# Optimization experiments

Hardware: AMD Instinct MI355X
Metric: run time of the kernel (lower is better)

The kernel has to match this reference:

```python
import jax, jax.numpy as jnp
import numpy as np

M, K, N = 4096, 7168, 18432  # tokens, in_features, out_features


def setup_inputs() -> dict:
    key = jax.random.key(0)
    kx, kw, ks = jax.random.split(key, 3)
    x = jax.random.normal(kx, (M, K), dtype=jnp.float32)
    # int8 quantized weight, layout [in_features, out_features] as in the torch module
    weight = jax.random.randint(kw, (K, N), -128, 128, dtype=jnp.int8)
    # per-output-channel dequant scale (bf16 in the original; fp32 here for a stable baseline)
    scale = jax.random.uniform(ks, (N,), dtype=jnp.float32) * 0.02 + 1e-3
    return {"x": x, "weight": weight, "scale": scale}


def reference(x, weight, scale):
    # Fused dequant + GEMM: y = x @ (int8_weight * scale_per_out_channel)
    w = weight.astype(x.dtype) * scale.astype(x.dtype)[None, :]  # [K, N]
    return x @ w  # [M, N]
```

## Files before the change

### kernel.cpp

```cpp
#include <hip/hip_runtime.h>
#include <hip/hip_bf16.h>
#include <cstdint>
#include <cstddef>

#define M_ 4096
#define K_ 7168
#define N_ 18432
#define NT 56
#define ITERS 28

typedef __attribute__((ext_vector_type(4))) int i32x4;

#define AS1 __attribute__((address_space(1)))
#define AS3 __attribute__((address_space(3)))

__device__ __forceinline__ void gld_lds16(void* lds, const void* g) {
  __builtin_amdgcn_global_load_lds((const AS1 void*)g, (AS3 void*)lds, 16, 0, 0);
}

__global__ __launch_bounds__(256) void quant_x_kernel(const float* __restrict__ x,
                                                      signed char* __restrict__ xq,
                                                      float* __restrict__ sx) {
  const int m = blockIdx.x;
  const float4* row4 = (const float4*)(x + (size_t)m * K_);
  float mx = 0.f;
  for (int i = threadIdx.x; i < K_ / 4; i += 256) {
    float4 v = row4[i];
    mx = fmaxf(mx, fmaxf(fmaxf(fabsf(v.x), fabsf(v.y)), fmaxf(fabsf(v.z), fabsf(v.w))));
  }
#pragma unroll
  for (int d = 1; d < 64; d <<= 1) mx = fmaxf(mx, __shfl_xor(mx, d));
  __shared__ float wred[4];
  if ((threadIdx.x & 63) == 0) wred[threadIdx.x >> 6] = mx;
  __syncthreads();
  mx = fmaxf(fmaxf(wred[0], wred[1]), fmaxf(wred[2], wred[3]));
  const float inv = mx > 0.f ? 127.f / mx : 0.f;
  if (threadIdx.x == 0) sx[m] = mx / 127.f;
  char4* q4 = (char4*)(xq + (size_t)m * K_);
  for (int i = threadIdx.x; i < K_ / 4; i += 256) {
    float4 v = row4[i];
    char4 c;
    c.x = (signed char)__float2int_rn(v.x * inv);
    c.y = (signed char)__float2int_rn(v.y * inv);
    c.z = (signed char)__float2int_rn(v.z * inv);
    c.w = (signed char)__float2int_rn(v.w * inv);
    q4[i] = c;
  }
}

__global__ __launch_bounds__(256) void transpose_w_kernel(const int* __restrict__ W,
                                                          signed char* __restrict__ Wt) {
  __shared__ __align__(16) signed char t[64][80];
  const int k0 = blockIdx.x * 64;
  const int n0 = blockIdx.y * 64;
  const int r = threadIdx.x >> 4;
  const int c4 = (threadIdx.x & 15) * 4;
#pragma unroll
  for (int rr = 0; rr < 4; ++rr) {
    const int row = rr * 16 + r;
    int4 v = *(const int4*)(W + (size_t)(k0 + row) * N_ + n0 + c4);
    t[c4 + 0][row] = (signed char)v.x;
    t[c4 + 1][row] = (signed char)v.y;
    t[c4 + 2][row] = (signed char)v.z;
    t[c4 + 3][row] = (signed char)v.w;
  }
  __syncthreads();
  const int nr = threadIdx.x >> 2;
  const int cb = (threadIdx.x & 3) * 16;
  int4 o = *(const int4*)&t[nr][cb];
  *(int4*)(Wt + (size_t)(n0 + nr) * K_ + k0 + cb) = o;
}

__global__ __launch_bounds__(512, 2) void gemm_i8_kernel(const signed char* __restrict__ Aq,
                                                         const signed char* __restrict__ Bt,
                                                         const float* __restrict__ sx,
                                                         const float* __restrict__ scale,
                                                         float* __restrict__ C) {
  __shared__ __align__(16) signed char lds[131072];

  const int NBN = 72;
  const int per = 144;
  const int bid = blockIdx.x;
  const int swz = (bid & 7) * per + (bid >> 3);
  const int m0 = (swz / NBN) * 256;
  const int n0 = (swz % NBN) * 256;

  const int tid = threadIdx.x;
  const int w = tid >> 6;
  const int lane = tid & 63;
  const int wr = w >> 2;
  const int wc = w & 3;

  const int fr = lane & 15;
  const int q = lane >> 4;
  const int sl = ((q ^ ((fr >> 1) & 3)) << 4);

  const int ls16 = (((lane & 3) ^ ((lane >> 3) & 3)) << 4);
  const int pr0 = w * 16 + (lane >> 2);
  const unsigned offA0 = (unsigned)(m0 + pr0) * K_ + ls16;
  const unsigned offA1 = (unsigned)(m0 + 128 + pr0) * K_ + ls16;
  const unsigned offB0 = (unsigned)(n0 + pr0) * K_ + ls16;
  const unsigned offB1 = (unsigned)(n0 + 128 + pr0) * K_ + ls16;

#define STAGE_A(T, KS) do {                                                        \
    const int tc_ = (T) < NT ? (T) : NT - 1;                                       \
    signed char* d_ = lds + (((T) & 1) * 32768 + (KS) * 16384 + w * 1024);         \
    gld_lds16(d_, Aq + (size_t)offA0 + tc_ * 128 + (KS) * 64);                     \
    gld_lds16(d_ + 8192, Aq + (size_t)offA1 + tc_ * 128 + (KS) * 64);              \
  } while (0)
#define STAGE_B(T, KS) do {                                                        \
    const int tc_ = (T) < NT ? (T) : NT - 1;                                       \
    signed char* d_ = lds + (65536 + ((T) & 1) * 32768 + (KS) * 16384 + w * 1024); \
    gld_lds16(d_, Bt + (size_t)offB0 + tc_ * 128 + (KS) * 64);                     \
    gld_lds16(d_ + 8192, Bt + (size_t)offB1 + tc_ * 128 + (KS) * 64);              \
  } while (0)
#define LDA(BUF, KS, MH) do {                                                      \
    const signed char* ab = lds + ((BUF) * 32768 + (KS) * 16384);                  \
    _Pragma("unroll") for (int i_ = 0; i_ < 4; ++i_)                               \
      aq[i_] = *(const i32x4*)(ab + (wr * 128 + ((MH) * 4 + i_) * 16 + fr) * 64 + sl); \
  } while (0)
#define LDB(BUF, KS) do {                                                          \
    const signed char* bb = lds + (65536 + (BUF) * 32768 + (KS) * 16384);          \
    _Pragma("unroll") for (int n_ = 0; n_ < 4; ++n_)                               \
      bq[n_] = *(const i32x4*)(bb + (wc * 64 + n_ * 16 + fr) * 64 + sl);           \
  } while (0)
#define MFMA16(MH) do {                                                            \
    __builtin_amdgcn_s_setprio(1);                                                 \
    _Pragma("unroll") for (int i_ = 0; i_ < 4; ++i_)                               \
    _Pragma("unroll") for (int n_ = 0; n_ < 4; ++n_)                               \
      acc[(MH) * 4 + i_][n_] = __builtin_amdgcn_mfma_i32_16x16x64_i8(              \
          aq[i_], bq[n_], acc[(MH) * 4 + i_][n_], 0, 0, 0);                        \
    __builtin_amdgcn_s_setprio(0);                                                 \
  } while (0)
#define FENCE asm volatile("" ::: "memory")
#define BAR do { FENCE; __builtin_amdgcn_s_barrier(); FENCE; } while (0)
#define LGKM0 asm volatile("s_waitcnt lgkmcnt(0)")
#define VM6 asm volatile("s_waitcnt vmcnt(6)")

  i32x4 acc[8][4] = {};
  i32x4 aq[4], bq[4];

  STAGE_B(0, 0); STAGE_A(0, 0); STAGE_B(0, 1); STAGE_A(0, 1);
  STAGE_B(1, 0); STAGE_A(1, 0); STAGE_B(1, 1);
  VM6;
  BAR;

  for (int it = 0; it < ITERS; ++it) {
    const int u = 2 * it;
    LDB(0, 0); LDA(0, 0, 0);
    STAGE_A(u + 1, 1);
    BAR; LGKM0;
    MFMA16(0);
    BAR;
    LDA(0, 0, 1);
    STAGE_B(u + 2, 0);
    BAR; LGKM0;
    MFMA16(1);
    BAR;
    LDB(0, 1); LDA(0, 1, 0);
    STAGE_A(u + 2, 0);
    BAR; LGKM0;
    MFMA16(0);
    BAR;
    LDA(0, 1, 1);
    STAGE_B(u + 2, 1);
    BAR; LGKM0;
    MFMA16(1);
    VM6;
    BAR;
    LDB(1, 0); LDA(1, 0, 0);
    STAGE_A(u + 2, 1);
    BAR; LGKM0;
    MFMA16(0);
    BAR;
    LDA(1, 0, 1);
    STAGE_B(u + 3, 0);
    BAR; LGKM0;
    MFMA16(1);
    BAR;
    LDB(1, 1); LDA(1, 1, 0);
    STAGE_A(u + 3, 0);
    BAR; LGKM0;
    MFMA16(0);
    BAR;
    LDA(1, 1, 1);
    STAGE_B(u + 3, 1);
    BAR; LGKM0;
    MFMA16(1);
    VM6;
    BAR;
  }

  const int mb = m0 + wr * 128;
  const int nb = n0 + wc * 64;
  const int col = lane & 15;
  const int rq = (lane >> 4) * 4;
  float scl[4];
#pragma unroll
  for (int n = 0; n < 4; ++n) scl[n] = scale[nb + n * 16 + col];
#pragma unroll
  for (int m = 0; m < 8; ++m) {
#pragma unroll
    for (int r = 0; r < 4; ++r) {
      const int row = mb + m * 16 + rq + r;
      const float s = sx[row];
      float* out = C + (size_t)row * N_ + nb + col;
#pragma unroll
      for (int n = 0; n < 4; ++n) out[n * 16] = (float)acc[m][n][r] * s * scl[n];
    }
  }
#undef STAGE_A
#undef STAGE_B
#undef LDA
#undef LDB
#undef MFMA16
#undef FENCE
#undef BAR
#undef LGKM0
#undef VM6
}

__global__ __launch_bounds__(256) void fb_gemm_kernel(const float* __restrict__ X,
                                                      const int* __restrict__ W,
                                                      const float* __restrict__ scale,
                                                      float* __restrict__ Y) {
  __shared__ float xs[16][65];
  __shared__ float ws_[16][65];
  const int bn = blockIdx.x * 64;
  const int bm = blockIdx.y * 64;
  const int tx = threadIdx.x & 15;
  const int ty = threadIdx.x >> 4;
  float acc[4][4] = {};
  for (int k0 = 0; k0 < K_; k0 += 16) {
    for (int i = threadIdx.x; i < 64 * 16; i += 256) {
      int r = i >> 4, c = i & 15;
      xs[c][r] = X[(size_t)(bm + r) * K_ + k0 + c];
    }
    for (int i = threadIdx.x; i < 16 * 64; i += 256) {
      int r = i >> 6, c = i & 63;
      ws_[r][c] = (float)W[(size_t)(k0 + r) * N_ + bn + c];
    }
    __syncthreads();
#pragma unroll
    for (int kk = 0; kk < 16; ++kk) {
      float a[4], b[4];
#pragma unroll
      for (int i = 0; i < 4; ++i) a[i] = xs[kk][ty * 4 + i];
#pragma unroll
      for (int j = 0; j < 4; ++j) b[j] = ws_[kk][tx * 4 + j];
#pragma unroll
      for (int i = 0; i < 4; ++i)
#pragma unroll
        for (int j = 0; j < 4; ++j) acc[i][j] += a[i] * b[j];
    }
    __syncthreads();
  }
#pragma unroll
  for (int i = 0; i < 4; ++i)
#pragma unroll
    for (int j = 0; j < 4; ++j)
      Y[(size_t)(bm + ty * 4 + i) * N_ + bn + tx * 4 + j] = acc[i][j] * scale[bn + tx * 4 + j];
}

extern "C" void kernel_launch(void* const* d_in, const int* in_sizes, int n_in,
                              void* d_out, int out_size, void* d_ws, size_t ws_size,
                              hipStream_t stream) {
  const float* x = (const float*)d_in[0];
  const int* w = (const int*)d_in[1];
  const float* scale = (const float*)d_in[2];
  float* y = (float*)d_out;

  const size_t xq_bytes = (size_t)M_ * K_;
  const size_t sx_off = xq_bytes;
  const size_t wt_off = sx_off + (size_t)M_ * 4;
  const size_t need = wt_off + (size_t)N_ * K_;

  if (ws_size >= need) {
    signed char* xq = (signed char*)d_ws;
    float* sx = (float*)((char*)d_ws + sx_off);
    signed char* wt = (signed char*)((char*)d_ws + wt_off);
    hipLaunchKernelGGL(quant_x_kernel, dim3(M_), dim3(256), 0, stream, x, xq, sx);
    hipLaunchKernelGGL(transpose_w_kernel, dim3(K_ / 64, N_ / 64), dim3(256), 0, stream, w, wt);
    hipLaunchKernelGGL(gemm_i8_kernel, dim3((M_ / 256) * (N_ / 256)), dim3(512), 0, stream,
                       xq, wt, sx, scale, y);
  } else {
    hipLaunchKernelGGL(fb_gemm_kernel, dim3(N_ / 64, M_ / 64), dim3(256), 0, stream,
                       x, w, scale, y);
  }
}
```

Baseline: 723.5 us.

## Double-buffer MFMA operand registers to overlap LDS reads with MFMA; remap XCD tiles

The int8 GEMM main loop now keeps two register sets for the A and B fragments. The LDS reads for the next sub-step are issued before the current MFMA batch, with sched_barrier fences in place of explicit lgkmcnt(0) waits, so LDS latency can hide behind matrix math. The block-to-tile mapping also changes so each XCD owns a contiguous group of N tiles and iterates over M within it, aiming for better L2 reuse of the weight tiles. This costs more VGPRs under launch bounds of 512 threads with 2 blocks per CU. It also relies on the compiler inserting correct waits across the barriers.

```diff
diff --git a/kernel.cpp b/kernel.cpp
--- a/kernel.cpp
+++ b/kernel.cpp
@@ -78,12 +78,11 @@
                                                          float* __restrict__ C) {
   __shared__ __align__(16) signed char lds[131072];
 
-  const int NBN = 72;
-  const int per = 144;
   const int bid = blockIdx.x;
-  const int swz = (bid & 7) * per + (bid >> 3);
-  const int m0 = (swz / NBN) * 256;
-  const int n0 = (swz % NBN) * 256;
+  const int xcd = bid & 7;
+  const int j = bid >> 3;
+  const int m0 = (j & 15) * 256;
+  const int n0 = (xcd * 9 + (j >> 4)) * 256;
 
   const int tid = threadIdx.x;
   const int w = tid >> 6;
@@ -114,80 +113,91 @@
     gld_lds16(d_, Bt + (size_t)offB0 + tc_ * 128 + (KS) * 64);                     \
     gld_lds16(d_ + 8192, Bt + (size_t)offB1 + tc_ * 128 + (KS) * 64);              \
   } while (0)
-#define LDA(BUF, KS, MH) do {                                                      \
+#define LDA_TO(DST, BUF, KS, MH) do {                                              \
     const signed char* ab = lds + ((BUF) * 32768 + (KS) * 16384);                  \
     _Pragma("unroll") for (int i_ = 0; i_ < 4; ++i_)                               \
-      aq[i_] = *(const i32x4*)(ab + (wr * 128 + ((MH) * 4 + i_) * 16 + fr) * 64 + sl); \
-  } while (0)
-#define LDB(BUF, KS) do {                                                          \
+      DST[i_] = *(const i32x4*)(ab + (wr * 128 + ((MH) * 4 + i_) * 16 + fr) * 64 + sl); \
+  } while (0)
+#define LDB_TO(DST, BUF, KS) do {                                                  \
     const signed char* bb = lds + (65536 + (BUF) * 32768 + (KS) * 16384);          \
     _Pragma("unroll") for (int n_ = 0; n_ < 4; ++n_)                               \
-      bq[n_] = *(const i32x4*)(bb + (wc * 64 + n_ * 16 + fr) * 64 + sl);           \
-  } while (0)
-#define MFMA16(MH) do {                                                            \
+      DST[n_] = *(const i32x4*)(bb + (wc * 64 + n_ * 16 + fr) * 64 + sl);          \
+  } while (0)
+#define MFMA16(MH, AQ, BQ) do {                                                    \
     __builtin_amdgcn_s_setprio(1);                                                 \
     _Pragma("unroll") for (int i_ = 0; i_ < 4; ++i_)                               \
     _Pragma("unroll") for (int n_ = 0; n_ < 4; ++n_)                               \
       acc[(MH) * 4 + i_][n_] = __builtin_amdgcn_mfma_i32_16x16x64_i8(              \
-          aq[i_], bq[n_], acc[(MH) * 4 + i_][n_], 0, 0, 0);                        \
+          AQ[i_], BQ[n_], acc[(MH) * 4 + i_][n_], 0, 0, 0);                        \
     __builtin_amdgcn_s_setprio(0);                                                 \
   } while (0)
 #define FENCE asm volatile("" ::: "memory")
 #define BAR do { FENCE; __builtin_amdgcn_s_barrier(); FENCE; } while (0)
-#define LGKM0 asm volatile("s_waitcnt lgkmcnt(0)")
-#define VM6 asm volatile("s_waitcnt vmcnt(6)")
+#define VM6 do { asm volatile("s_waitcnt vmcnt(6)" ::: "memory"); \
+                 __builtin_amdgcn_sched_barrier(0); } while (0)
+#define SB __builtin_amdgcn_sched_barrier(0)
 
   i32x4 acc[8][4] = {};
-  i32x4 aq[4], bq[4];
+  i32x4 aq0[4], aq1[4], bq0[4], bq1[4];
 
   STAGE_B(0, 0); STAGE_A(0, 0); STAGE_B(0, 1); STAGE_A(0, 1);
   STAGE_B(1, 0); STAGE_A(1, 0); STAGE_B(1, 1);
   VM6;
   BAR;
+  LDB_TO(bq0, 0, 0); LDA_TO(aq0, 0, 0, 0);
+  SB;
 
   for (int it = 0; it < ITERS; ++it) {
     const int u = 2 * it;
-    LDB(0, 0); LDA(0, 0, 0);
     STAGE_A(u + 1, 1);
-    BAR; LGKM0;
-    MFMA16(0);
-    BAR;
-    LDA(0, 0, 1);
+    BAR;
+    LDA_TO(aq1, 0, 0, 1);
+    SB;
+    MFMA16(0, aq0, bq0);
+    BAR;
     STAGE_B(u + 2, 0);
-    BAR; LGKM0;
-    MFMA16(1);
-    BAR;
-    LDB(0, 1); LDA(0, 1, 0);
+    BAR;
+    LDB_TO(bq1, 0, 1); LDA_TO(aq0, 0, 1, 0);
+    SB;
+    MFMA16(1, aq1, bq0);
+    BAR;
     STAGE_A(u + 2, 0);
-    BAR; LGKM0;
-    MFMA16(0);
-    BAR;
-    LDA(0, 1, 1);
+    BAR;
+    LDA_TO(aq1, 0, 1, 1);
+    SB;
+    MFMA16(0, aq0, bq1);
+    BAR;
     STAGE_B(u + 2, 1);
-    BAR; LGKM0;
-    MFMA16(1);
+    BAR;
     VM6;
-    BAR;
-    LDB(1, 0); LDA(1, 0, 0);
+    LDB_TO(bq0, 1, 0); LDA_TO(aq0, 1, 0, 0);
+    SB;
+    MFMA16(1, aq1, bq1);
+    BAR;
     STAGE_A(u + 2, 1);
-    BAR; LGKM0;
-    MFMA16(0);
-    BAR;
-    LDA(1, 0, 1);
+    BAR;
+    LDA_TO(aq1, 1, 0, 1);
+    SB;
+    MFMA16(0, aq0, bq0);
+    BAR;
     STAGE_B(u + 3, 0);
-    BAR; LGKM0;
-    MFMA16(1);
-    BAR;
-    LDB(1, 1); LDA(1, 1, 0);
+    BAR;
+    LDB_TO(bq1, 1, 1); LDA_TO(aq0, 1, 1, 0);
+    SB;
+    MFMA16(1, aq1, bq0);
+    BAR;
     STAGE_A(u + 3, 0);
-    BAR; LGKM0;
-    MFMA16(0);
-    BAR;
-    LDA(1, 1, 1);
+    BAR;
+    LDA_TO(aq1, 1, 1, 1);
+    SB;
+    MFMA16(0, aq0, bq1);
+    BAR;
     STAGE_B(u + 3, 1);
-    BAR; LGKM0;
-    MFMA16(1);
+    BAR;
     VM6;
+    LDB_TO(bq0, 0, 0); LDA_TO(aq0, 0, 0, 0);
+    SB;
+    MFMA16(1, aq1, bq1);
     BAR;
   }
 
@@ -211,13 +221,13 @@
   }
 #undef STAGE_A
 #undef STAGE_B
-#undef LDA
-#undef LDB
+#undef LDA_TO
+#undef LDB_TO
 #undef MFMA16
 #undef FENCE
 #undef BAR
-#undef LGKM0
 #undef VM6
+#undef SB
 }
 
 __global__ __launch_bounds__(256) void fb_gemm_kernel(const float* __restrict__ X,
```

Measured after the change: 725.2 us. Within noise of the previous version (+0.2%).
